# Performance work log

Hardware: AMD Instinct MI355X
Metric: run time of the kernel (lower is better)

The kernel has to match this reference:

```python
import jax, jax.numpy as jnp
import numpy as np

D_MODEL = 128
N_HEAD = 6
D_HEAD = D_MODEL // N_HEAD  # 21
D_CAT = N_HEAD * D_HEAD     # 126 (note: != d_model, matches torch source)
D_FF = 4 * D_MODEL
EPS = 1e-5


def setup_inputs() -> dict:
    key = jax.random.key(0)
    ks = jax.random.split(key, 12)
    B, T = 512, 128
    s = 0.02
    return {
        "x":  jax.random.normal(ks[0], (B, T, D_MODEL), dtype=jnp.float32),
        "Wq": jax.random.normal(ks[1], (N_HEAD, D_MODEL, D_HEAD), dtype=jnp.float32) * s,
        "Wk": jax.random.normal(ks[2], (N_HEAD, D_MODEL, D_HEAD), dtype=jnp.float32) * s,
        "Wv": jax.random.normal(ks[3], (N_HEAD, D_MODEL, D_HEAD), dtype=jnp.float32) * s,
        "Wo": jax.random.normal(ks[4], (D_CAT, D_MODEL), dtype=jnp.float32) * s,
        "bo": jnp.zeros((D_MODEL,), dtype=jnp.float32),
        "W1": jax.random.normal(ks[5], (D_MODEL, D_FF), dtype=jnp.float32) * s,
        "b1": jnp.zeros((D_FF,), dtype=jnp.float32),
        "W2": jax.random.normal(ks[6], (D_FF, D_MODEL), dtype=jnp.float32) * s,
        "b2": jnp.zeros((D_MODEL,), dtype=jnp.float32),
        "g1": jnp.ones((D_MODEL,), dtype=jnp.float32),
        "beta1": jnp.zeros((D_MODEL,), dtype=jnp.float32),
        "g2": jnp.ones((D_MODEL,), dtype=jnp.float32),
        "beta2": jnp.zeros((D_MODEL,), dtype=jnp.float32),
    }


def _layernorm(x, g, b):
    mu = jnp.mean(x, axis=-1, keepdims=True)
    var = jnp.mean(jnp.square(x - mu), axis=-1, keepdims=True)
    return (x - mu) * jax.lax.rsqrt(var + EPS) * g + b


def reference(x, Wq, Wk, Wv, Wo, bo, W1, b1, W2, b2, g1, beta1, g2, beta2):
    B, T, _ = x.shape
    # --- masked multi-head self-attention on ln1(x) (pre-norm), dropout = eval/identity ---
    h = _layernorm(x, g1, beta1)
    q = jnp.einsum('btd,hde->bhte', h, Wq)
    k = jnp.einsum('btd,hde->bhte', h, Wk)
    v = jnp.einsum('btd,hde->bhte', h, Wv)
    scores = jnp.einsum('bhte,bhse->bhts', q, k) / jnp.sqrt(jnp.float32(D_HEAD))
    causal = jnp.tril(jnp.ones((T, T), dtype=bool))  # tril buffer, T x T
    scores = jnp.where(causal, scores, jnp.float32(-jnp.inf))
    a = jax.nn.softmax(scores, axis=-1)
    o = jnp.einsum('bhts,bhse->bhte', a, v)
    o = o.transpose(0, 2, 1, 3).reshape(B, T, D_CAT)  # concat heads -> 126
    x = x + (o @ Wo + bo)
    # --- feed-forward on ln2(x) ---
    h2 = _layernorm(x, g2, beta2)
    ff = jax.nn.relu(h2 @ W1 + b1) @ W2 + b2
    return x + ff
```

## Files before the change

kernel.cpp:

```cpp
#include <hip/hip_runtime.h>
#include <math.h>

typedef short short8 __attribute__((ext_vector_type(8)));
typedef float f32x4 __attribute__((ext_vector_type(4)));

constexpr int B_ = 512, T_ = 128, D_ = 128, H_ = 6, E_ = 21, DC_ = 126, F_ = 512;
constexpr float EPS_ = 1e-5f;

__device__ __forceinline__ short f2bf(float f) {
    unsigned u = __float_as_uint(f);
    u = (u + 0x7FFFu + ((u >> 16) & 1u)) >> 16;
    return (short)u;
}
__device__ __forceinline__ unsigned pk2(float lo, float hi) {
    return (unsigned)(unsigned short)f2bf(lo) | ((unsigned)(unsigned short)f2bf(hi) << 16);
}
__device__ __forceinline__ f32x4 mfma16(short8 a, short8 b, f32x4 c) {
    return __builtin_amdgcn_mfma_f32_16x16x32_bf16(a, b, c, 0, 0, 0);
}

__global__ __launch_bounds__(256) void prep_kernel(
    const float* __restrict__ Wq, const float* __restrict__ Wk, const float* __restrict__ Wv,
    const float* __restrict__ Wo, const float* __restrict__ W1, const float* __restrict__ W2,
    short* __restrict__ WcatT, short* __restrict__ W1T, short* __restrict__ W2T,
    short* __restrict__ WoT) {
    int idx = blockIdx.x * 256 + threadIdx.x;
    if (idx < 49152) {
        int n = idx >> 7, k = idx & 127;
        float v = 0.f;
        if (n < 378) {
            int w = n / 126, r = n % 126, hd = r / 21, e = r % 21;
            const float* src = (w == 0) ? Wq : (w == 1) ? Wk : Wv;
            v = src[(hd * 128 + k) * 21 + e];
        }
        WcatT[idx] = f2bf(v);
    } else if (idx < 114688) {
        int i = idx - 49152;
        int j = i >> 7, d = i & 127;
        W1T[i] = f2bf(W1[d * 512 + j]);
    } else if (idx < 180224) {
        int i = idx - 114688;
        int d = i >> 9, j = i & 511;
        W2T[i] = f2bf(W2[j * 128 + d]);
    } else if (idx < 196608) {
        int i = idx - 180224;
        int d = i >> 7, c = i & 127;
        WoT[i] = f2bf(c < 126 ? Wo[c * 128 + d] : 0.f);
    }
}

__global__ __launch_bounds__(512) void qkv_kernel(
    const float* __restrict__ x, const float* __restrict__ g1, const float* __restrict__ be1,
    const short* __restrict__ WcatT,
    short* __restrict__ Qg, short* __restrict__ Kg, short* __restrict__ VTg) {
    __shared__ __align__(16) short hA[T_ * D_];
    int b = blockIdx.x, tid = threadIdx.x;
    const f32x4 fzero = {0.f, 0.f, 0.f, 0.f};
    {
        int r = tid >> 2, q = tid & 3;
        const float* xr = x + ((size_t)b * T_ + r) * D_ + q * 32;
        float vals[32];
        float sum = 0.f, sq = 0.f;
        #pragma unroll
        for (int i = 0; i < 8; ++i) {
            f32x4 v4 = *(const f32x4*)(xr + i * 4);
            #pragma unroll
            for (int j = 0; j < 4; ++j) { float vv = v4[j]; vals[i*4+j] = vv; sum += vv; sq += vv*vv; }
        }
        sum += __shfl_xor(sum, 1); sum += __shfl_xor(sum, 2);
        sq  += __shfl_xor(sq, 1);  sq  += __shfl_xor(sq, 2);
        float mu = sum * (1.f / 128.f);
        float rs = rsqrtf(sq * (1.f / 128.f) - mu * mu + EPS_);
        char* hb = (char*)hA;
        #pragma unroll
        for (int cc = 0; cc < 4; ++cc) {
            short8 pk;
            #pragma unroll
            for (int j = 0; j < 8; ++j) {
                int d0 = q * 32 + cc * 8 + j;
                pk[j] = f2bf((vals[cc*8+j] - mu) * rs * g1[d0] + be1[d0]);
            }
            int byte = (r * 256 + q * 64 + cc * 16) ^ ((r & 7) << 4);
            *(short8*)(hb + byte) = pk;
        }
    }
    __syncthreads();
    int lane = tid & 63, wid = tid >> 6;
    int wm = wid >> 2, wn = wid & 3;
    int rlo = lane & 15, khi = lane >> 4;
    f32x4 acc[4][6];
    #pragma unroll
    for (int m = 0; m < 4; ++m)
        #pragma unroll
        for (int n = 0; n < 6; ++n) acc[m][n] = fzero;
    const char* hb = (const char*)hA;
    #pragma unroll
    for (int ks = 0; ks < 4; ++ks) {
        short8 a[4];
        #pragma unroll
        for (int m = 0; m < 4; ++m) {
            int row = (wm * 4 + m) * 16 + rlo;
            int byte = (row * 256 + ks * 64 + khi * 16) ^ ((row & 7) << 4);
            a[m] = *(const short8*)(hb + byte);
        }
        #pragma unroll
        for (int n = 0; n < 6; ++n) {
            int col = (wn * 6 + n) * 16 + rlo;
            short8 bfr = *(const short8*)(WcatT + col * 128 + ks * 32 + khi * 8);
            #pragma unroll
            for (int m = 0; m < 4; ++m) acc[m][n] = mfma16(a[m], bfr, acc[m][n]);
        }
    }
    #pragma unroll
    for (int m = 0; m < 4; ++m) {
        #pragma unroll
        for (int n = 0; n < 6; ++n) {
            int ng = (wn * 6 + n) * 16 + rlo;
            if (ng < 378) {
                int w = ng / 126, r2 = ng % 126;
                int hd = r2 / 21, e = r2 % 21;
                size_t bh = (size_t)b * 6 + hd;
                #pragma unroll
                for (int reg = 0; reg < 4; ++reg) {
                    int t = (wm * 4 + m) * 16 + khi * 4 + reg;
                    short bv = f2bf(acc[m][n][reg]);
                    if (w == 0)      Qg[(bh * 128 + t) * 32 + e] = bv;
                    else if (w == 1) Kg[(bh * 128 + t) * 32 + e] = bv;
                    else             VTg[(bh * 32 + e) * 128 + t] = bv;
                }
            }
        }
    }
}

__global__ __launch_bounds__(256) void attn_kernel(
    const short* __restrict__ Qg, const short* __restrict__ Kg, const short* __restrict__ VTg,
    short* __restrict__ Obf) {
    __shared__ __align__(16) short Qs[T_ * 32];
    __shared__ __align__(16) short Ks[T_ * 32];
    __shared__ __align__(16) short VTs[32 * T_];
    __shared__ __align__(16) short Ps[T_ * T_];
    int h = blockIdx.x, b = blockIdx.y, tid = threadIdx.x;
    size_t bh = (size_t)b * 6 + h;
    const f32x4 fzero = {0.f, 0.f, 0.f, 0.f};
    {
        char* qb = (char*)Qs; char* kb = (char*)Ks;
        const short* Qsrc = Qg + bh * (128 * 32);
        const short* Ksrc = Kg + bh * (128 * 32);
        for (int c = tid; c < 512; c += 256) {
            int r = c >> 2, cc = c & 3;
            int byte = (r * 64 + cc * 16) ^ ((r & 3) << 4);
            short8 qv = {0,0,0,0,0,0,0,0}, kv = {0,0,0,0,0,0,0,0};
            if (cc < 3) {
                qv = *(const short8*)(Qsrc + r * 32 + cc * 8);
                kv = *(const short8*)(Ksrc + r * 32 + cc * 8);
                if (cc == 2) {
                    qv[5] = 0; qv[6] = 0; qv[7] = 0;
                    kv[5] = 0; kv[6] = 0; kv[7] = 0;
                }
            }
            *(short8*)(qb + byte) = qv;
            *(short8*)(kb + byte) = kv;
        }
        char* vb = (char*)VTs;
        const short* Vsrc = VTg + bh * (32 * 128);
        for (int c = tid; c < 512; c += 256) {
            int e = c >> 4, cc = c & 15;
            short8 vv = {0,0,0,0,0,0,0,0};
            if (e < 21) vv = *(const short8*)(Vsrc + e * 128 + cc * 8);
            int byte = (e * 256 + cc * 16) ^ ((e & 7) << 4);
            *(short8*)(vb + byte) = vv;
        }
        short8 z = {0,0,0,0,0,0,0,0};
        char* pb = (char*)Ps;
        for (int c = tid; c < 2048; c += 256) *(short8*)(pb + c * 16) = z;
    }
    __syncthreads();
    int lane = tid & 63, wid = tid >> 6;
    int rlo = lane & 15, khi = lane >> 4;
    const float scale = 0.2182178902359924f;
    const char* qb = (const char*)Qs;
    const char* kb = (const char*)Ks;
    char* pb = (char*)Ps;
    #pragma unroll
    for (int pass = 0; pass < 2; ++pass) {
        int Mt = wid + pass * 4;
        int arow = Mt * 16 + rlo;
        short8 a = *(const short8*)(qb + ((arow * 64 + khi * 16) ^ ((arow & 3) << 4)));
        f32x4 sacc[8];
        #pragma unroll
        for (int nt = 0; nt < 8; ++nt) {
            sacc[nt] = fzero;
            if (nt <= Mt) {
                int brow = nt * 16 + rlo;
                short8 bf = *(const short8*)(kb + ((brow * 64 + khi * 16) ^ ((brow & 3) << 4)));
                sacc[nt] = mfma16(a, bf, sacc[nt]);
            }
        }
        #pragma unroll
        for (int reg = 0; reg < 4; ++reg) {
            int t = Mt * 16 + khi * 4 + reg;
            float m = -3e38f;
            #pragma unroll
            for (int nt = 0; nt < 8; ++nt) {
                if (nt <= Mt) {
                    int s = nt * 16 + rlo;
                    float v = (s <= t) ? sacc[nt][reg] * scale : -3e38f;
                    sacc[nt][reg] = v;
                    m = fmaxf(m, v);
                }
            }
            m = fmaxf(m, __shfl_xor(m, 1));
            m = fmaxf(m, __shfl_xor(m, 2));
            m = fmaxf(m, __shfl_xor(m, 4));
            m = fmaxf(m, __shfl_xor(m, 8));
            float sum = 0.f;
            #pragma unroll
            for (int nt = 0; nt < 8; ++nt) {
                if (nt <= Mt) {
                    float p = __expf(sacc[nt][reg] - m);
                    sacc[nt][reg] = p;
                    sum += p;
                }
            }
            sum += __shfl_xor(sum, 1);
            sum += __shfl_xor(sum, 2);
            sum += __shfl_xor(sum, 4);
            sum += __shfl_xor(sum, 8);
            float inv = 1.f / sum;
            #pragma unroll
            for (int nt = 0; nt < 8; ++nt) {
                if (nt <= Mt) {
                    int s = nt * 16 + rlo;
                    int byte = (t * 256 + s * 2) ^ ((t & 7) << 4);
                    *(short*)(pb + byte) = f2bf(sacc[nt][reg] * inv);
                }
            }
        }
    }
    __syncthreads();
    const char* vb = (const char*)VTs;
    #pragma unroll
    for (int pass = 0; pass < 2; ++pass) {
        int Mt = wid + pass * 4;
        f32x4 oacc0 = fzero, oacc1 = fzero;
        int ksmax = Mt >> 1;
        for (int ks = 0; ks <= ksmax; ++ks) {
            int arow = Mt * 16 + rlo;
            int kof = ks * 64 + khi * 16;
            short8 a = *(const short8*)(pb + ((arow * 256 + kof) ^ ((arow & 7) << 4)));
            int er0 = rlo;
            short8 b0 = *(const short8*)(vb + ((er0 * 256 + kof) ^ ((er0 & 7) << 4)));
            oacc0 = mfma16(a, b0, oacc0);
            int er1 = 16 + rlo;
            short8 b1v = *(const short8*)(vb + ((er1 * 256 + kof) ^ ((er1 & 7) << 4)));
            oacc1 = mfma16(a, b1v, oacc1);
        }
        #pragma unroll
        for (int reg = 0; reg < 4; ++reg) {
            int t = Mt * 16 + khi * 4 + reg;
            int e0 = rlo;
            Obf[((size_t)b * 128 + t) * 128 + h * 21 + e0] = f2bf(oacc0[reg]);
            int e1 = 16 + rlo;
            if (e1 < 21)
                Obf[((size_t)b * 128 + t) * 128 + h * 21 + e1] = f2bf(oacc1[reg]);
        }
    }
}

__global__ __launch_bounds__(256) void proj_kernel(
    const float* __restrict__ x, const short* __restrict__ Obf, const short* __restrict__ WoT,
    const float* __restrict__ bo, float* __restrict__ out) {
    __shared__ __align__(16) short Os[64 * 128];
    int r0 = blockIdx.x * 64, tid = threadIdx.x;
    const f32x4 fzero = {0.f, 0.f, 0.f, 0.f};
    char* ob = (char*)Os;
    for (int c = tid; c < 1024; c += 256) {
        int r = c >> 4, cc = c & 15;
        short8 v = *(const short8*)(Obf + (size_t)(r0 + r) * 128 + cc * 8);
        if (cc == 15) { v[6] = 0; v[7] = 0; }
        int byte = (r * 256 + cc * 16) ^ ((r & 7) << 4);
        *(short8*)(ob + byte) = v;
    }
    __syncthreads();
    int lane = tid & 63, mt = tid >> 6;
    int rlo = lane & 15, khi = lane >> 4;
    #pragma unroll
    for (int nt = 0; nt < 8; ++nt) {
        int d = nt * 16 + rlo;
        f32x4 acc = fzero;
        #pragma unroll
        for (int ks = 0; ks < 4; ++ks) {
            int arow = mt * 16 + rlo;
            short8 a = *(const short8*)(ob + ((arow * 256 + ks * 64 + khi * 16) ^ ((arow & 7) << 4)));
            short8 bf = *(const short8*)(WoT + d * 128 + ks * 32 + khi * 8);
            acc = mfma16(a, bf, acc);
        }
        float bod = bo[d];
        #pragma unroll
        for (int reg = 0; reg < 4; ++reg) {
            int row = r0 + mt * 16 + khi * 4 + reg;
            out[(size_t)row * 128 + d] = x[(size_t)row * 128 + d] + bod + acc[reg];
        }
    }
}

__global__ __launch_bounds__(256, 2) void ff_kernel(
    float* __restrict__ out, const float* __restrict__ g2, const float* __restrict__ be2,
    const short* __restrict__ W1T, const float* __restrict__ b1,
    const short* __restrict__ W2T, const float* __restrict__ b2) {
    __shared__ __align__(16) short Hs[64 * 128];
    __shared__ __align__(16) short Fs[64 * 512];
    int tid = threadIdx.x;
    int lane = tid & 63, wid = tid >> 6;
    int rlo = lane & 15, khi = lane >> 4;
    int rowbase = blockIdx.x * 64;
    const f32x4 fzero = {0.f, 0.f, 0.f, 0.f};
    {
        int rl = lane >> 2, q = lane & 3;
        int r = wid * 16 + rl;
        const float* xr = out + (size_t)(rowbase + r) * D_ + q * 32;
        float vals[32];
        float sum = 0.f, sq = 0.f;
        #pragma unroll
        for (int i = 0; i < 8; ++i) {
            f32x4 v4 = *(const f32x4*)(xr + i * 4);
            #pragma unroll
            for (int j = 0; j < 4; ++j) { float vv = v4[j]; vals[i*4+j] = vv; sum += vv; sq += vv*vv; }
        }
        sum += __shfl_xor(sum, 1); sum += __shfl_xor(sum, 2);
        sq  += __shfl_xor(sq, 1);  sq  += __shfl_xor(sq, 2);
        float mu = sum * (1.f / 128.f);
        float rs = rsqrtf(sq * (1.f / 128.f) - mu * mu + EPS_);
        char* hb = (char*)Hs;
        #pragma unroll
        for (int cc = 0; cc < 4; ++cc) {
            short8 pk;
            #pragma unroll
            for (int j = 0; j < 8; ++j) {
                int d0 = q * 32 + cc * 8 + j;
                pk[j] = f2bf((vals[cc*8+j] - mu) * rs * g2[d0] + be2[d0]);
            }
            int byte = (r * 256 + q * 64 + cc * 16) ^ ((r & 7) << 4);
            *(short8*)(hb + byte) = pk;
        }
    }
    __syncthreads();
    short8 hfr[4][4];
    {
        const char* hb = (const char*)Hs;
        #pragma unroll
        for (int mt = 0; mt < 4; ++mt)
            #pragma unroll
            for (int kk = 0; kk < 4; ++kk) {
                int t = mt * 16 + rlo;
                hfr[mt][kk] = *(const short8*)(hb + ((t * 256 + kk * 64 + khi * 16) ^ ((t & 7) << 4)));
            }
    }
    {
        const short* W1w = W1T + (size_t)(wid * 128) * 128;
        char* fb = (char*)Fs;
        #pragma unroll 2
        for (int jt = 0; jt < 8; ++jt) {
            f32x4 fa[4];
            #pragma unroll
            for (int mt = 0; mt < 4; ++mt) fa[mt] = fzero;
            #pragma unroll
            for (int kk = 0; kk < 4; ++kk) {
                short8 wa = *(const short8*)(W1w + (size_t)(jt * 16 + rlo) * 128 + kk * 32 + khi * 8);
                #pragma unroll
                for (int mt = 0; mt < 4; ++mt) fa[mt] = mfma16(wa, hfr[mt][kk], fa[mt]);
            }
            f32x4 bq = *(const f32x4*)(b1 + wid * 128 + jt * 16 + khi * 4);
            #pragma unroll
            for (int mt = 0; mt < 4; ++mt) {
                float v0 = fmaxf(fa[mt][0] + bq[0], 0.f);
                float v1 = fmaxf(fa[mt][1] + bq[1], 0.f);
                float v2 = fmaxf(fa[mt][2] + bq[2], 0.f);
                float v3 = fmaxf(fa[mt][3] + bq[3], 0.f);
                uint2 w;
                w.x = pk2(v0, v1);
                w.y = pk2(v2, v3);
                int t = mt * 16 + rlo;
                int byte = (t * 1024 + wid * 256 + jt * 32 + khi * 8) ^ ((t & 7) << 4);
                *(uint2*)(fb + byte) = w;
            }
        }
    }
    __syncthreads();
    f32x4 oa[4][2];
    #pragma unroll
    for (int mt = 0; mt < 4; ++mt) { oa[mt][0] = fzero; oa[mt][1] = fzero; }
    {
        const char* fb = (const char*)Fs;
        const short* W2w = W2T + (size_t)(wid * 32) * 512;
        #pragma unroll 4
        for (int ks = 0; ks < 16; ++ks) {
            short8 af[4];
            #pragma unroll
            for (int mt = 0; mt < 4; ++mt) {
                int t = mt * 16 + rlo;
                af[mt] = *(const short8*)(fb + ((t * 1024 + ks * 64 + khi * 16) ^ ((t & 7) << 4)));
            }
            #pragma unroll
            for (int nd = 0; nd < 2; ++nd) {
                short8 wf = *(const short8*)(W2w + (size_t)(nd * 16 + rlo) * 512 + ks * 32 + khi * 8);
                #pragma unroll
                for (int mt = 0; mt < 4; ++mt) oa[mt][nd] = mfma16(af[mt], wf, oa[mt][nd]);
            }
        }
    }
    #pragma unroll
    for (int nd = 0; nd < 2; ++nd) {
        int d = wid * 32 + nd * 16 + rlo;
        float b2d = b2[d];
        #pragma unroll
        for (int mt = 0; mt < 4; ++mt) {
            #pragma unroll
            for (int reg = 0; reg < 4; ++reg) {
                int row = rowbase + mt * 16 + khi * 4 + reg;
                size_t gi = (size_t)row * D_ + d;
                out[gi] = out[gi] + b2d + oa[mt][nd][reg];
            }
        }
    }
}

extern "C" void kernel_launch(void* const* d_in, const int* in_sizes, int n_in,
                              void* d_out, int out_size, void* d_ws, size_t ws_size,
                              hipStream_t stream) {
    const float* x   = (const float*)d_in[0];
    const float* Wq  = (const float*)d_in[1];
    const float* Wk  = (const float*)d_in[2];
    const float* Wv  = (const float*)d_in[3];
    const float* Wo  = (const float*)d_in[4];
    const float* bo  = (const float*)d_in[5];
    const float* W1  = (const float*)d_in[6];
    const float* b1  = (const float*)d_in[7];
    const float* W2  = (const float*)d_in[8];
    const float* b2  = (const float*)d_in[9];
    const float* g1  = (const float*)d_in[10];
    const float* be1 = (const float*)d_in[11];
    const float* g2  = (const float*)d_in[12];
    const float* be2 = (const float*)d_in[13];
    float* out = (float*)d_out;

    char* wsb = (char*)d_ws;
    short* WcatT = (short*)(wsb);
    short* W1T   = (short*)(wsb + 98304);
    short* W2T   = (short*)(wsb + 229376);
    short* WoT   = (short*)(wsb + 360448);
    short* Qg    = (short*)(wsb + 393216);
    short* Kg    = (short*)(wsb + 25559040);
    short* VTg   = (short*)(wsb + 50724864);
    short* Obf   = (short*)(wsb + 75890688);

    prep_kernel<<<768, 256, 0, stream>>>(Wq, Wk, Wv, Wo, W1, W2, WcatT, W1T, W2T, WoT);
    qkv_kernel<<<512, 512, 0, stream>>>(x, g1, be1, WcatT, Qg, Kg, VTg);
    attn_kernel<<<dim3(6, 512), 256, 0, stream>>>(Qg, Kg, VTg, Obf);
    proj_kernel<<<1024, 256, 0, stream>>>(x, Obf, WoT, bo, out);
    ff_kernel<<<1024, 256, 0, stream>>>(out, g2, be2, W1T, b1, W2T, b2);
}
```

Measured before the change: 278.1 us.

## Pad QKV heads to 32 columns, vectorize stores, and fuse attention softmax with PV

The concatenated QKV weight is padded so each head occupies 32 columns with zeros beyond 21. This lets the QKV kernel store Q and K as packed 8-byte rows, and V transposed, instead of scattered scalar writes. Q/K use a swapped MFMA operand order so the accumulator layout matches the row-major stores. The attention kernel now reads Q fragments straight from global memory and drops the LDS zero-fill of P. It computes the softmax in the transposed layout with exp2 (log2e folded into the scale) and does PV right after each wave's own rows, removing a block barrier. Pass ordering is balanced across waves. The change relies on the padded columns being zero in the workspace, and the per-wave P reuse depends on each wave reading only the P rows it wrote.

```diff
diff --git a/kernel.cpp b/kernel.cpp
--- a/kernel.cpp
+++ b/kernel.cpp
@@ -25,25 +25,27 @@
     short* __restrict__ WcatT, short* __restrict__ W1T, short* __restrict__ W2T,
     short* __restrict__ WoT) {
     int idx = blockIdx.x * 256 + threadIdx.x;
-    if (idx < 49152) {
+    if (idx < 73728) {
         int n = idx >> 7, k = idx & 127;
+        int w = (n >= 384) ? 2 : (n >= 192 ? 1 : 0);
+        int rem = n - w * 192;
+        int hd = rem >> 5, e = rem & 31;
         float v = 0.f;
-        if (n < 378) {
-            int w = n / 126, r = n % 126, hd = r / 21, e = r % 21;
+        if (e < 21) {
             const float* src = (w == 0) ? Wq : (w == 1) ? Wk : Wv;
             v = src[(hd * 128 + k) * 21 + e];
         }
         WcatT[idx] = f2bf(v);
-    } else if (idx < 114688) {
-        int i = idx - 49152;
+    } else if (idx < 139264) {
+        int i = idx - 73728;
         int j = i >> 7, d = i & 127;
         W1T[i] = f2bf(W1[d * 512 + j]);
-    } else if (idx < 180224) {
-        int i = idx - 114688;
+    } else if (idx < 204800) {
+        int i = idx - 139264;
         int d = i >> 9, j = i & 511;
         W2T[i] = f2bf(W2[j * 128 + d]);
-    } else if (idx < 196608) {
-        int i = idx - 180224;
+    } else if (idx < 221184) {
+        int i = idx - 204800;
         int d = i >> 7, c = i & 127;
         WoT[i] = f2bf(c < 126 ? Wo[c * 128 + d] : 0.f);
     }
@@ -88,46 +90,62 @@
     int lane = tid & 63, wid = tid >> 6;
     int wm = wid >> 2, wn = wid & 3;
     int rlo = lane & 15, khi = lane >> 4;
-    f32x4 acc[4][6];
+    f32x4 acc[4][9];
     #pragma unroll
     for (int m = 0; m < 4; ++m)
         #pragma unroll
-        for (int n = 0; n < 6; ++n) acc[m][n] = fzero;
+        for (int j = 0; j < 9; ++j) acc[m][j] = fzero;
     const char* hb = (const char*)hA;
     #pragma unroll
     for (int ks = 0; ks < 4; ++ks) {
-        short8 a[4];
+        short8 hfr[4];
         #pragma unroll
         for (int m = 0; m < 4; ++m) {
             int row = (wm * 4 + m) * 16 + rlo;
-            int byte = (row * 256 + ks * 64 + khi * 16) ^ ((row & 7) << 4);
-            a[m] = *(const short8*)(hb + byte);
-        }
-        #pragma unroll
-        for (int n = 0; n < 6; ++n) {
-            int col = (wn * 6 + n) * 16 + rlo;
-            short8 bfr = *(const short8*)(WcatT + col * 128 + ks * 32 + khi * 8);
-            #pragma unroll
-            for (int m = 0; m < 4; ++m) acc[m][n] = mfma16(a[m], bfr, acc[m][n]);
-        }
-    }
-    #pragma unroll
-    for (int m = 0; m < 4; ++m) {
-        #pragma unroll
-        for (int n = 0; n < 6; ++n) {
-            int ng = (wn * 6 + n) * 16 + rlo;
-            if (ng < 378) {
-                int w = ng / 126, r2 = ng % 126;
-                int hd = r2 / 21, e = r2 % 21;
-                size_t bh = (size_t)b * 6 + hd;
+            hfr[m] = *(const short8*)(hb + ((row * 256 + ks * 64 + khi * 16) ^ ((row & 7) << 4)));
+        }
+        #pragma unroll
+        for (int j = 0; j < 9; ++j) {
+            int nt = wn * 9 + j;
+            short8 wf = *(const short8*)(WcatT + (size_t)(nt * 16 + rlo) * 128 + ks * 32 + khi * 8);
+            if (nt < 24) {
                 #pragma unroll
-                for (int reg = 0; reg < 4; ++reg) {
-                    int t = (wm * 4 + m) * 16 + khi * 4 + reg;
-                    short bv = f2bf(acc[m][n][reg]);
-                    if (w == 0)      Qg[(bh * 128 + t) * 32 + e] = bv;
-                    else if (w == 1) Kg[(bh * 128 + t) * 32 + e] = bv;
-                    else             VTg[(bh * 32 + e) * 128 + t] = bv;
-                }
+                for (int m = 0; m < 4; ++m) acc[m][j] = mfma16(wf, hfr[m], acc[m][j]);
+            } else {
+                #pragma unroll
+                for (int m = 0; m < 4; ++m) acc[m][j] = mfma16(hfr[m], wf, acc[m][j]);
+            }
+        }
+    }
+    #pragma unroll
+    for (int j = 0; j < 9; ++j) {
+        int nt = wn * 9 + j;
+        if (nt < 24) {
+            int ng = nt * 16 + khi * 4;
+            int w = (ng >= 192) ? 1 : 0;
+            int hd = (ng >> 5) - w * 6;
+            int e32 = ng & 31;
+            short* dst = (w ? Kg : Qg) + (((size_t)b * 6 + hd) * 128) * 32 + e32;
+            #pragma unroll
+            for (int m = 0; m < 4; ++m) {
+                int t = (wm * 4 + m) * 16 + rlo;
+                uint2 pv;
+                pv.x = pk2(acc[m][j][0], acc[m][j][1]);
+                pv.y = pk2(acc[m][j][2], acc[m][j][3]);
+                *(uint2*)(dst + (size_t)t * 32) = pv;
+            }
+        } else {
+            int ng = nt * 16 + rlo;
+            int hd = (ng >> 5) - 12;
+            int e32 = ng & 31;
+            short* dst = VTg + (((size_t)b * 6 + hd) * 32 + e32) * 128;
+            #pragma unroll
+            for (int m = 0; m < 4; ++m) {
+                int t0 = (wm * 4 + m) * 16 + khi * 4;
+                uint2 pv;
+                pv.x = pk2(acc[m][j][0], acc[m][j][1]);
+                pv.y = pk2(acc[m][j][2], acc[m][j][3]);
+                *(uint2*)(dst + t0) = pv;
             }
         }
     }
@@ -136,7 +154,6 @@
 __global__ __launch_bounds__(256) void attn_kernel(
     const short* __restrict__ Qg, const short* __restrict__ Kg, const short* __restrict__ VTg,
     short* __restrict__ Obf) {
-    __shared__ __align__(16) short Qs[T_ * 32];
     __shared__ __align__(16) short Ks[T_ * 32];
     __shared__ __align__(16) short VTs[32 * T_];
     __shared__ __align__(16) short Ps[T_ * T_];
@@ -144,126 +161,93 @@
     size_t bh = (size_t)b * 6 + h;
     const f32x4 fzero = {0.f, 0.f, 0.f, 0.f};
     {
-        char* qb = (char*)Qs; char* kb = (char*)Ks;
-        const short* Qsrc = Qg + bh * (128 * 32);
+        char* kb = (char*)Ks;
         const short* Ksrc = Kg + bh * (128 * 32);
+        #pragma unroll
         for (int c = tid; c < 512; c += 256) {
             int r = c >> 2, cc = c & 3;
-            int byte = (r * 64 + cc * 16) ^ ((r & 3) << 4);
-            short8 qv = {0,0,0,0,0,0,0,0}, kv = {0,0,0,0,0,0,0,0};
-            if (cc < 3) {
-                qv = *(const short8*)(Qsrc + r * 32 + cc * 8);
-                kv = *(const short8*)(Ksrc + r * 32 + cc * 8);
-                if (cc == 2) {
-                    qv[5] = 0; qv[6] = 0; qv[7] = 0;
-                    kv[5] = 0; kv[6] = 0; kv[7] = 0;
-                }
-            }
-            *(short8*)(qb + byte) = qv;
-            *(short8*)(kb + byte) = kv;
+            *(short8*)(kb + ((r * 64 + cc * 16) ^ ((r & 3) << 4))) =
+                *(const short8*)(Ksrc + r * 32 + cc * 8);
         }
         char* vb = (char*)VTs;
         const short* Vsrc = VTg + bh * (32 * 128);
+        #pragma unroll
         for (int c = tid; c < 512; c += 256) {
             int e = c >> 4, cc = c & 15;
-            short8 vv = {0,0,0,0,0,0,0,0};
-            if (e < 21) vv = *(const short8*)(Vsrc + e * 128 + cc * 8);
-            int byte = (e * 256 + cc * 16) ^ ((e & 7) << 4);
-            *(short8*)(vb + byte) = vv;
-        }
-        short8 z = {0,0,0,0,0,0,0,0};
-        char* pb = (char*)Ps;
-        for (int c = tid; c < 2048; c += 256) *(short8*)(pb + c * 16) = z;
+            *(short8*)(vb + ((e * 256 + cc * 16) ^ ((e & 7) << 4))) =
+                *(const short8*)(Vsrc + e * 128 + cc * 8);
+        }
     }
     __syncthreads();
     int lane = tid & 63, wid = tid >> 6;
     int rlo = lane & 15, khi = lane >> 4;
-    const float scale = 0.2182178902359924f;
-    const char* qb = (const char*)Qs;
+    const float s2 = 0.31482188f;
     const char* kb = (const char*)Ks;
+    const char* vb = (const char*)VTs;
     char* pb = (char*)Ps;
     #pragma unroll
     for (int pass = 0; pass < 2; ++pass) {
-        int Mt = wid + pass * 4;
-        int arow = Mt * 16 + rlo;
-        short8 a = *(const short8*)(qb + ((arow * 64 + khi * 16) ^ ((arow & 3) << 4)));
+        int Mt = (pass == 0) ? wid : 7 - wid;
+        int t = Mt * 16 + rlo;
+        short8 qf = *(const short8*)(Qg + (bh * 128 + t) * 32 + khi * 8);
         f32x4 sacc[8];
         #pragma unroll
-        for (int nt = 0; nt < 8; ++nt) {
-            sacc[nt] = fzero;
-            if (nt <= Mt) {
-                int brow = nt * 16 + rlo;
-                short8 bf = *(const short8*)(kb + ((brow * 64 + khi * 16) ^ ((brow & 3) << 4)));
-                sacc[nt] = mfma16(a, bf, sacc[nt]);
-            }
+        for (int St = 0; St < 8; ++St) {
+            sacc[St] = fzero;
+            if (St <= Mt) {
+                int srow = St * 16 + rlo;
+                short8 kf = *(const short8*)(kb + ((srow * 64 + khi * 16) ^ ((srow & 3) << 4)));
+                sacc[St] = mfma16(kf, qf, sacc[St]);
+            }
+        }
+        float m = -3e38f;
+        #pragma unroll
+        for (int St = 0; St < 8; ++St)
+            #pragma unroll
+            for (int reg = 0; reg < 4; ++reg) {
+                int s = St * 16 + khi * 4 + reg;
+                float v = (s <= t) ? sacc[St][reg] * s2 : -3e38f;
+                sacc[St][reg] = v;
+                m = fmaxf(m, v);
+            }
+        m = fmaxf(m, __shfl_xor(m, 16));
+        m = fmaxf(m, __shfl_xor(m, 32));
+        float sum = 0.f;
+        #pragma unroll
+        for (int St = 0; St < 8; ++St)
+            #pragma unroll
+            for (int reg = 0; reg < 4; ++reg) {
+                float p = exp2f(sacc[St][reg] - m);
+                sacc[St][reg] = p;
+                sum += p;
+            }
+        sum += __shfl_xor(sum, 16);
+        sum += __shfl_xor(sum, 32);
+        float inv = 1.f / sum;
+        #pragma unroll
+        for (int St = 0; St < 8; ++St) {
+            uint2 pv;
+            pv.x = pk2(sacc[St][0] * inv, sacc[St][1] * inv);
+            pv.y = pk2(sacc[St][2] * inv, sacc[St][3] * inv);
+            *(uint2*)(pb + ((t * 256 + St * 32 + khi * 8) ^ ((t & 7) << 4))) = pv;
+        }
+        f32x4 o0 = fzero, o1 = fzero;
+        int kmax = Mt >> 1;
+        for (int ks = 0; ks <= kmax; ++ks) {
+            int kof = ks * 64 + khi * 16;
+            int arow = Mt * 16 + rlo;
+            short8 pa = *(const short8*)(pb + ((arow * 256 + kof) ^ ((arow & 7) << 4)));
+            short8 b0 = *(const short8*)(vb + ((rlo * 256 + kof) ^ ((rlo & 7) << 4)));
+            short8 b1v = *(const short8*)(vb + (((16 + rlo) * 256 + kof) ^ (((16 + rlo) & 7) << 4)));
+            o0 = mfma16(pa, b0, o0);
+            o1 = mfma16(pa, b1v, o1);
         }
         #pragma unroll
         for (int reg = 0; reg < 4; ++reg) {
-            int t = Mt * 16 + khi * 4 + reg;
-            float m = -3e38f;
-            #pragma unroll
-            for (int nt = 0; nt < 8; ++nt) {
-                if (nt <= Mt) {
-                    int s = nt * 16 + rlo;
-                    float v = (s <= t) ? sacc[nt][reg] * scale : -3e38f;
-                    sacc[nt][reg] = v;
-                    m = fmaxf(m, v);
-                }
-            }
-            m = fmaxf(m, __shfl_xor(m, 1));
-            m = fmaxf(m, __shfl_xor(m, 2));
-            m = fmaxf(m, __shfl_xor(m, 4));
-            m = fmaxf(m, __shfl_xor(m, 8));
-            float sum = 0.f;
-            #pragma unroll
-            for (int nt = 0; nt < 8; ++nt) {
-                if (nt <= Mt) {
-                    float p = __expf(sacc[nt][reg] - m);
-                    sacc[nt][reg] = p;
-                    sum += p;
-                }
-            }
-            sum += __shfl_xor(sum, 1);
-            sum += __shfl_xor(sum, 2);
-            sum += __shfl_xor(sum, 4);
-            sum += __shfl_xor(sum, 8);
-            float inv = 1.f / sum;
-            #pragma unroll
-            for (int nt = 0; nt < 8; ++nt) {
-                if (nt <= Mt) {
-                    int s = nt * 16 + rlo;
-                    int byte = (t * 256 + s * 2) ^ ((t & 7) << 4);
-                    *(short*)(pb + byte) = f2bf(sacc[nt][reg] * inv);
-                }
-            }
-        }
-    }
-    __syncthreads();
-    const char* vb = (const char*)VTs;
-    #pragma unroll
-    for (int pass = 0; pass < 2; ++pass) {
-        int Mt = wid + pass * 4;
-        f32x4 oacc0 = fzero, oacc1 = fzero;
-        int ksmax = Mt >> 1;
-        for (int ks = 0; ks <= ksmax; ++ks) {
-            int arow = Mt * 16 + rlo;
-            int kof = ks * 64 + khi * 16;
-            short8 a = *(const short8*)(pb + ((arow * 256 + kof) ^ ((arow & 7) << 4)));
-            int er0 = rlo;
-            short8 b0 = *(const short8*)(vb + ((er0 * 256 + kof) ^ ((er0 & 7) << 4)));
-            oacc0 = mfma16(a, b0, oacc0);
-            int er1 = 16 + rlo;
-            short8 b1v = *(const short8*)(vb + ((er1 * 256 + kof) ^ ((er1 & 7) << 4)));
-            oacc1 = mfma16(a, b1v, oacc1);
-        }
-        #pragma unroll
-        for (int reg = 0; reg < 4; ++reg) {
-            int t = Mt * 16 + khi * 4 + reg;
-            int e0 = rlo;
-            Obf[((size_t)b * 128 + t) * 128 + h * 21 + e0] = f2bf(oacc0[reg]);
-            int e1 = 16 + rlo;
-            if (e1 < 21)
-                Obf[((size_t)b * 128 + t) * 128 + h * 21 + e1] = f2bf(oacc1[reg]);
+            int t2 = Mt * 16 + khi * 4 + reg;
+            Obf[((size_t)b * 128 + t2) * 128 + h * 21 + rlo] = f2bf(o0[reg]);
+            if (rlo < 5)
+                Obf[((size_t)b * 128 + t2) * 128 + h * 21 + 16 + rlo] = f2bf(o1[reg]);
         }
     }
 }
@@ -447,15 +431,15 @@
 
     char* wsb = (char*)d_ws;
     short* WcatT = (short*)(wsb);
-    short* W1T   = (short*)(wsb + 98304);
-    short* W2T   = (short*)(wsb + 229376);
-    short* WoT   = (short*)(wsb + 360448);
-    short* Qg    = (short*)(wsb + 393216);
-    short* Kg    = (short*)(wsb + 25559040);
-    short* VTg   = (short*)(wsb + 50724864);
-    short* Obf   = (short*)(wsb + 75890688);
-
-    prep_kernel<<<768, 256, 0, stream>>>(Wq, Wk, Wv, Wo, W1, W2, WcatT, W1T, W2T, WoT);
+    short* W1T   = (short*)(wsb + 147456);
+    short* W2T   = (short*)(wsb + 278528);
+    short* WoT   = (short*)(wsb + 409600);
+    short* Qg    = (short*)(wsb + 442368);
+    short* Kg    = (short*)(wsb + 25608192);
+    short* VTg   = (short*)(wsb + 50774016);
+    short* Obf   = (short*)(wsb + 75939840);
+
+    prep_kernel<<<864, 256, 0, stream>>>(Wq, Wk, Wv, Wo, W1, W2, WcatT, W1T, W2T, WoT);
     qkv_kernel<<<512, 512, 0, stream>>>(x, g1, be1, WcatT, Qg, Kg, VTg);
     attn_kernel<<<dim3(6, 512), 256, 0, stream>>>(Qg, Kg, VTg, Obf);
     proj_kernel<<<1024, 256, 0, stream>>>(x, Obf, WoT, bo, out);
```

Result: no change. 283.5 us (+1.9%).
